# Kernel optimization log

Measured on AMD Instinct MI355X. Metric: run time of the kernel, lower is better.

The kernel has to match this reference:

```python
import jax, jax.numpy as jnp
import numpy as np


def setup_inputs() -> dict:
    key = jax.random.key(0)
    kx, kw = jax.random.split(key)
    x = jax.random.normal(kx, (8192, 4096), dtype=jnp.float32)
    weight = jax.random.normal(kw, (4096, 4096), dtype=jnp.float32)  # [out, in]
    return {"x": x, "weight": weight}


def reference(x, weight):
    sg = jax.lax.stop_gradient
    # --- ternary weight quantization with STE ---
    abs_mean = sg(jnp.mean(jnp.abs(weight)))           # detached scalar
    threshold = 0.7 * abs_mean
    w_quant = jnp.where(jnp.abs(weight) < threshold, 0.0, jnp.sign(weight))
    non_zero_mean = jnp.mean((w_quant != 0).astype(weight.dtype)) + 1e-8
    scale_w = abs_mean / non_zero_mean
    w_scaled = w_quant * scale_w
    w_ste = sg(w_scaled - weight) + weight
    # --- int8 activation quantization with STE ---
    q_max = 127.0
    x_abs_max = sg(jnp.max(jnp.abs(x)))
    scale_x = q_max / jnp.maximum(x_abs_max, 1e-12)    # guard div-by-zero; if x==0, output==0 anyway
    x_dequant = jnp.round(x * scale_x) / scale_x
    x_ste = sg(x_dequant - x) + x
    # --- full-precision GEMM on fake-quantized operands ---
    return jnp.einsum('ti,oi->to', x_ste, w_ste)  # [tokens, out]
```

## Files before the change

### kernel.cpp

```cpp
#include <hip/hip_runtime.h>
#include <stdint.h>


#define M_DIM 8192
#define N_DIM 4096
#define K_DIM 4096
#define W_ELEMS (N_DIM * K_DIM)
#define X_ELEMS (M_DIM * K_DIM)

typedef int   int4v   __attribute__((ext_vector_type(4)));
typedef float float4v __attribute__((ext_vector_type(4)));

#define WS_ABSMEAN 0
#define WS_SCALEX  4
#define WS_THR     8
#define WS_CS      16
#define WS_WSUM    64
#define WS_XMAX    16384
#define WS_NZ      24576
#define WS_WQ_OFF  32768
#define WS_XQ_OFF  (32768 + W_ELEMS)

__global__ __launch_bounds__(256) void pass1(const float4v* __restrict__ w,
                                             const float4v* __restrict__ x,
                                             uint8_t* ws) {
    const int tid = threadIdx.x;
    __shared__ double lsd[4];
    __shared__ float lsf[4];
    if (blockIdx.x < 1024) {
        int idx = blockIdx.x * 256 + tid;
        double s = 0.0;
#pragma unroll 4
        for (int it = 0; it < 16; ++it) {
            float4v v = w[idx + it * 262144];
            s += (double)fabsf(v.x) + (double)fabsf(v.y) + (double)fabsf(v.z) + (double)fabsf(v.w);
        }
        for (int off = 32; off > 0; off >>= 1) s += __shfl_down(s, off);
        if ((tid & 63) == 0) lsd[tid >> 6] = s;
        __syncthreads();
        if (tid == 0) ((double*)(ws + WS_WSUM))[blockIdx.x] = lsd[0] + lsd[1] + lsd[2] + lsd[3];
    } else {
        int b = blockIdx.x - 1024;
        int idx = b * 256 + tid;
        float m = 0.0f;
#pragma unroll 4
        for (int it = 0; it < 16; ++it) {
            float4v v = x[idx + it * 524288];
            m = fmaxf(m, fmaxf(fmaxf(fabsf(v.x), fabsf(v.y)), fmaxf(fabsf(v.z), fabsf(v.w))));
        }
        for (int off = 32; off > 0; off >>= 1) m = fmaxf(m, __shfl_down(m, off));
        if ((tid & 63) == 0) lsf[tid >> 6] = m;
        __syncthreads();
        if (tid == 0) ((float*)(ws + WS_XMAX))[b] = fmaxf(fmaxf(lsf[0], lsf[1]), fmaxf(lsf[2], lsf[3]));
    }
}

__global__ __launch_bounds__(256) void pass2(uint8_t* ws) {
    const int tid = threadIdx.x;
    const double* wp = (const double*)(ws + WS_WSUM);
    const float* xp = (const float*)(ws + WS_XMAX);
    double s = wp[tid] + wp[tid + 256] + wp[tid + 512] + wp[tid + 768];
    float m = 0.0f;
#pragma unroll
    for (int j = 0; j < 8; ++j) m = fmaxf(m, xp[tid + j * 256]);
    for (int off = 32; off > 0; off >>= 1) {
        s += __shfl_down(s, off);
        m = fmaxf(m, __shfl_down(m, off));
    }
    __shared__ double lsd[4];
    __shared__ float lsf[4];
    if ((tid & 63) == 0) { lsd[tid >> 6] = s; lsf[tid >> 6] = m; }
    __syncthreads();
    if (tid == 0) {
        double tot = lsd[0] + lsd[1] + lsd[2] + lsd[3];
        float maxAbs = fmaxf(fmaxf(lsf[0], lsf[1]), fmaxf(lsf[2], lsf[3]));
        float abs_mean = (float)(tot * (1.0 / 16777216.0));
        *(float*)(ws + WS_ABSMEAN) = abs_mean;
        *(float*)(ws + WS_SCALEX) = 127.0f / fmaxf(maxAbs, 1e-12f);
        *(float*)(ws + WS_THR) = 0.7f * abs_mean;
    }
}

__global__ __launch_bounds__(256) void quant(const float4v* __restrict__ w,
                                             const float4v* __restrict__ x,
                                             uint8_t* ws) {
    const int tid = threadIdx.x;
    uint32_t* wq = (uint32_t*)(ws + WS_WQ_OFF);
    uint32_t* xq = (uint32_t*)(ws + WS_XQ_OFF);
    if (blockIdx.x < 1024) {
        const float thr = *(const float*)(ws + WS_THR);
        int idx = blockIdx.x * 256 + tid;
        int nz = 0;
        for (int it = 0; it < 16; ++it) {
            int i = idx + it * 262144;
            float4v v = w[i];
            uint32_t pk = 0;
#pragma unroll
            for (int c = 0; c < 4; ++c) {
                float f = v[c];
                int q = (fabsf(f) < thr) ? 0 : (f > 0.0f ? 1 : -1);
                nz += (q != 0);
                pk |= (uint32_t)(q & 0xff) << (8 * c);
            }
            wq[i] = pk;
        }
        for (int off = 32; off > 0; off >>= 1) nz += __shfl_down(nz, off);
        __shared__ int lsn[4];
        if ((tid & 63) == 0) lsn[tid >> 6] = nz;
        __syncthreads();
        if (tid == 0) ((int*)(ws + WS_NZ))[blockIdx.x] = lsn[0] + lsn[1] + lsn[2] + lsn[3];
    } else {
        const float sx = *(const float*)(ws + WS_SCALEX);
        int b = blockIdx.x - 1024;
        int idx = b * 256 + tid;
        for (int it = 0; it < 16; ++it) {
            int i = idx + it * 524288;
            float4v v = x[i];
            uint32_t pk = 0;
#pragma unroll
            for (int c = 0; c < 4; ++c) {
                int q = (int)rintf(v[c] * sx);
                pk |= (uint32_t)(q & 0xff) << (8 * c);
            }
            xq[i] = pk;
        }
    }
}

__global__ __launch_bounds__(256) void pass3(uint8_t* ws) {
    const int tid = threadIdx.x;
    const int* np = (const int*)(ws + WS_NZ);
    int s = np[tid] + np[tid + 256] + np[tid + 512] + np[tid + 768];
    for (int off = 32; off > 0; off >>= 1) s += __shfl_down(s, off);
    __shared__ int ls[4];
    if ((tid & 63) == 0) ls[tid >> 6] = s;
    __syncthreads();
    if (tid == 0) {
        float nzm = (float)(ls[0] + ls[1] + ls[2] + ls[3]) * (1.0f / 16777216.0f) + 1e-8f;
        float abs_mean = *(const float*)(ws + WS_ABSMEAN);
        float sx = *(const float*)(ws + WS_SCALEX);
        *(float*)(ws + WS_CS) = (abs_mean / nzm) / sx;
    }
}

__device__ __forceinline__ void load16_to_lds(const void* gsrc, void* ldst) {
    __builtin_amdgcn_global_load_lds(
        (const __attribute__((address_space(1))) uint32_t*)gsrc,
        (__attribute__((address_space(3))) uint32_t*)ldst, 16, 0, 0);
}

__global__ __launch_bounds__(256) void gemm_i8(const int8_t* __restrict__ Aq,
                                               const int8_t* __restrict__ Bq,
                                               float* __restrict__ out,
                                               const uint8_t* __restrict__ ws) {
    __shared__ int8_t lds[32768];
    int8_t* ldsA = lds;
    int8_t* ldsB = lds + 16384;

    int bid = blockIdx.x;
    int cpx = gridDim.x >> 3;
    int swz = (bid & 7) * cpx + (bid >> 3);
    int bm = swz / (N_DIM / 128);
    int bn = swz % (N_DIM / 128);

    const int tid = threadIdx.x;
    const int lane = tid & 63;
    const int w = tid >> 6;
    const int wr = w >> 1, wc = w & 1;

    const int8_t* Abase = Aq + (size_t)bm * 128 * K_DIM;
    const int8_t* Bbase = Bq + (size_t)bn * 128 * K_DIM;

    int4v acc[4][4] = {};

    for (int kt = 0; kt < K_DIM; kt += 128) {
        __syncthreads();
#pragma unroll
        for (int i = 0; i < 4; ++i) {
            int p = i * 4096 + tid * 16;
            int r = p >> 7;
            int s = (p >> 4) & 7;
            int q = s ^ (r & 7);
            load16_to_lds(Abase + (size_t)r * K_DIM + kt + q * 16, ldsA + p);
            load16_to_lds(Bbase + (size_t)r * K_DIM + kt + q * 16, ldsB + p);
        }
        __syncthreads();

#pragma unroll
        for (int kh = 0; kh < 2; ++kh) {
            int4v af[4], bf[4];
            const int qq = kh * 4 + (lane >> 4);
#pragma unroll
            for (int m = 0; m < 4; ++m) {
                int rowA = wr * 64 + m * 16 + (lane & 15);
                af[m] = *(const int4v*)(ldsA + rowA * 128 + ((qq ^ (rowA & 7)) << 4));
            }
#pragma unroll
            for (int n = 0; n < 4; ++n) {
                int rowB = wc * 64 + n * 16 + (lane & 15);
                bf[n] = *(const int4v*)(ldsB + rowB * 128 + ((qq ^ (rowB & 7)) << 4));
            }
#pragma unroll
            for (int m = 0; m < 4; ++m)
#pragma unroll
                for (int n = 0; n < 4; ++n)
                    acc[m][n] = __builtin_amdgcn_mfma_i32_16x16x64_i8(af[m], bf[n], acc[m][n], 0, 0, 0);
        }
    }

    const float cs = *(const float*)(ws + WS_CS);

    const int orow0 = bm * 128 + wr * 64 + (lane >> 4) * 4;
    const int ocol0 = bn * 128 + wc * 64 + (lane & 15);
#pragma unroll
    for (int m = 0; m < 4; ++m)
#pragma unroll
        for (int n = 0; n < 4; ++n)
#pragma unroll
            for (int j = 0; j < 4; ++j) {
                int row = orow0 + m * 16 + j;
                int col = ocol0 + n * 16;
                out[(size_t)row * N_DIM + col] = (float)acc[m][n][j] * cs;
            }
}

extern "C" void kernel_launch(void* const* d_in, const int* in_sizes, int n_in,
                              void* d_out, int out_size, void* d_ws, size_t ws_size,
                              hipStream_t stream) {
    const float4v* x = (const float4v*)d_in[0];
    const float4v* wgt = (const float4v*)d_in[1];
    float* out = (float*)d_out;
    uint8_t* ws = (uint8_t*)d_ws;
    int8_t* wq = (int8_t*)(ws + WS_WQ_OFF);
    int8_t* xq = (int8_t*)(ws + WS_XQ_OFF);

    pass1<<<3072, 256, 0, stream>>>(wgt, x, ws);
    pass2<<<1, 256, 0, stream>>>(ws);
    quant<<<3072, 256, 0, stream>>>(wgt, x, ws);
    pass3<<<1, 256, 0, stream>>>(ws);
    gemm_i8<<<2048, 256, 0, stream>>>(xq, wq, out, ws);
}
```

Before: 488.3 us.

## Enlarge GEMM tiles, double-buffer LDS, and fold scalar reductions into consumer kernels

The int8 GEMM moves from 128x128 tiles with 256 threads to 256x256 tiles with 512 threads. K-tiles are double-buffered in LDS, prefetching the next tile while computing the current one, and MFMA bursts are bracketed with barriers and s_setprio. The two single-block scalar kernels are removed: each quant block re-reduces the per-block partials to get its threshold or scale, and each GEMM block recomputes the output scale. This removes launches and serialization and raises data reuse per tile, at the cost of redundant small reductions in every block and 128KB LDS per block, which limits occupancy.

```diff
diff --git a/kernel.cpp b/kernel.cpp
--- a/kernel.cpp
+++ b/kernel.cpp
@@ -5,94 +5,79 @@
 #define M_DIM 8192
 #define N_DIM 4096
 #define K_DIM 4096
-#define W_ELEMS (N_DIM * K_DIM)
-#define X_ELEMS (M_DIM * K_DIM)
 
 typedef int   int4v   __attribute__((ext_vector_type(4)));
 typedef float float4v __attribute__((ext_vector_type(4)));
 
-#define WS_ABSMEAN 0
-#define WS_SCALEX  4
-#define WS_THR     8
-#define WS_CS      16
-#define WS_WSUM    64
-#define WS_XMAX    16384
-#define WS_NZ      24576
-#define WS_WQ_OFF  32768
-#define WS_XQ_OFF  (32768 + W_ELEMS)
-
-__global__ __launch_bounds__(256) void pass1(const float4v* __restrict__ w,
-                                             const float4v* __restrict__ x,
-                                             uint8_t* ws) {
+#define WS_WSUM 64
+#define WS_XMAX 16448
+#define WS_NZ   32832
+#define WS_WQ   65536
+#define WS_XQ   (65536 + N_DIM * K_DIM)
+
+__global__ __launch_bounds__(256) void reduce_k(const float4v* __restrict__ w,
+                                                const float4v* __restrict__ x,
+                                                uint8_t* ws) {
     const int tid = threadIdx.x;
     __shared__ double lsd[4];
     __shared__ float lsf[4];
-    if (blockIdx.x < 1024) {
+    if (blockIdx.x < 2048) {
         int idx = blockIdx.x * 256 + tid;
-        double s = 0.0;
-#pragma unroll 4
-        for (int it = 0; it < 16; ++it) {
-            float4v v = w[idx + it * 262144];
-            s += (double)fabsf(v.x) + (double)fabsf(v.y) + (double)fabsf(v.z) + (double)fabsf(v.w);
-        }
+        double s0 = 0.0, s1 = 0.0;
+#pragma unroll
+        for (int it = 0; it < 8; it += 2) {
+            float4v a = w[idx + it * 524288];
+            float4v b = w[idx + (it + 1) * 524288];
+            s0 += (double)((fabsf(a.x) + fabsf(a.y)) + (fabsf(a.z) + fabsf(a.w)));
+            s1 += (double)((fabsf(b.x) + fabsf(b.y)) + (fabsf(b.z) + fabsf(b.w)));
+        }
+        double s = s0 + s1;
         for (int off = 32; off > 0; off >>= 1) s += __shfl_down(s, off);
         if ((tid & 63) == 0) lsd[tid >> 6] = s;
         __syncthreads();
         if (tid == 0) ((double*)(ws + WS_WSUM))[blockIdx.x] = lsd[0] + lsd[1] + lsd[2] + lsd[3];
     } else {
-        int b = blockIdx.x - 1024;
-        int idx = b * 256 + tid;
-        float m = 0.0f;
-#pragma unroll 4
-        for (int it = 0; it < 16; ++it) {
-            float4v v = x[idx + it * 524288];
-            m = fmaxf(m, fmaxf(fmaxf(fabsf(v.x), fabsf(v.y)), fmaxf(fabsf(v.z), fabsf(v.w))));
-        }
+        int idx = (blockIdx.x - 2048) * 256 + tid;
+        float m0 = 0.0f, m1 = 0.0f;
+#pragma unroll
+        for (int it = 0; it < 8; it += 2) {
+            float4v a = x[idx + it * 1048576];
+            float4v b = x[idx + (it + 1) * 1048576];
+            m0 = fmaxf(m0, fmaxf(fmaxf(fabsf(a.x), fabsf(a.y)), fmaxf(fabsf(a.z), fabsf(a.w))));
+            m1 = fmaxf(m1, fmaxf(fmaxf(fabsf(b.x), fabsf(b.y)), fmaxf(fabsf(b.z), fabsf(b.w))));
+        }
+        float m = fmaxf(m0, m1);
         for (int off = 32; off > 0; off >>= 1) m = fmaxf(m, __shfl_down(m, off));
         if ((tid & 63) == 0) lsf[tid >> 6] = m;
         __syncthreads();
-        if (tid == 0) ((float*)(ws + WS_XMAX))[b] = fmaxf(fmaxf(lsf[0], lsf[1]), fmaxf(lsf[2], lsf[3]));
-    }
-}
-
-__global__ __launch_bounds__(256) void pass2(uint8_t* ws) {
+        if (tid == 0)
+            ((float*)(ws + WS_XMAX))[blockIdx.x - 2048] = fmaxf(fmaxf(lsf[0], lsf[1]), fmaxf(lsf[2], lsf[3]));
+    }
+}
+
+__global__ __launch_bounds__(256) void quant_k(const float4v* __restrict__ w,
+                                               const float4v* __restrict__ x,
+                                               uint8_t* ws) {
     const int tid = threadIdx.x;
-    const double* wp = (const double*)(ws + WS_WSUM);
-    const float* xp = (const float*)(ws + WS_XMAX);
-    double s = wp[tid] + wp[tid + 256] + wp[tid + 512] + wp[tid + 768];
-    float m = 0.0f;
-#pragma unroll
-    for (int j = 0; j < 8; ++j) m = fmaxf(m, xp[tid + j * 256]);
-    for (int off = 32; off > 0; off >>= 1) {
-        s += __shfl_down(s, off);
-        m = fmaxf(m, __shfl_down(m, off));
-    }
     __shared__ double lsd[4];
     __shared__ float lsf[4];
-    if ((tid & 63) == 0) { lsd[tid >> 6] = s; lsf[tid >> 6] = m; }
-    __syncthreads();
-    if (tid == 0) {
-        double tot = lsd[0] + lsd[1] + lsd[2] + lsd[3];
-        float maxAbs = fmaxf(fmaxf(lsf[0], lsf[1]), fmaxf(lsf[2], lsf[3]));
-        float abs_mean = (float)(tot * (1.0 / 16777216.0));
-        *(float*)(ws + WS_ABSMEAN) = abs_mean;
-        *(float*)(ws + WS_SCALEX) = 127.0f / fmaxf(maxAbs, 1e-12f);
-        *(float*)(ws + WS_THR) = 0.7f * abs_mean;
-    }
-}
-
-__global__ __launch_bounds__(256) void quant(const float4v* __restrict__ w,
-                                             const float4v* __restrict__ x,
-                                             uint8_t* ws) {
-    const int tid = threadIdx.x;
-    uint32_t* wq = (uint32_t*)(ws + WS_WQ_OFF);
-    uint32_t* xq = (uint32_t*)(ws + WS_XQ_OFF);
-    if (blockIdx.x < 1024) {
-        const float thr = *(const float*)(ws + WS_THR);
+    __shared__ int lsn[4];
+    if (blockIdx.x < 2048) {
+        const double* wp = (const double*)(ws + WS_WSUM);
+        double s = 0.0;
+#pragma unroll
+        for (int j = 0; j < 8; ++j) s += wp[tid + j * 256];
+        for (int off = 32; off > 0; off >>= 1) s += __shfl_down(s, off);
+        if ((tid & 63) == 0) lsd[tid >> 6] = s;
+        __syncthreads();
+        const float thr = 0.7f * (float)((lsd[0] + lsd[1] + lsd[2] + lsd[3]) * (1.0 / 16777216.0));
+
+        uint32_t* wq = (uint32_t*)(ws + WS_WQ);
         int idx = blockIdx.x * 256 + tid;
         int nz = 0;
-        for (int it = 0; it < 16; ++it) {
-            int i = idx + it * 262144;
+#pragma unroll
+        for (int it = 0; it < 8; ++it) {
+            int i = idx + it * 524288;
             float4v v = w[i];
             uint32_t pk = 0;
 #pragma unroll
@@ -105,16 +90,25 @@
             wq[i] = pk;
         }
         for (int off = 32; off > 0; off >>= 1) nz += __shfl_down(nz, off);
-        __shared__ int lsn[4];
         if ((tid & 63) == 0) lsn[tid >> 6] = nz;
         __syncthreads();
         if (tid == 0) ((int*)(ws + WS_NZ))[blockIdx.x] = lsn[0] + lsn[1] + lsn[2] + lsn[3];
     } else {
-        const float sx = *(const float*)(ws + WS_SCALEX);
-        int b = blockIdx.x - 1024;
-        int idx = b * 256 + tid;
-        for (int it = 0; it < 16; ++it) {
-            int i = idx + it * 524288;
+        const float* xp = (const float*)(ws + WS_XMAX);
+        float m = 0.0f;
+#pragma unroll
+        for (int j = 0; j < 16; ++j) m = fmaxf(m, xp[tid + j * 256]);
+        for (int off = 32; off > 0; off >>= 1) m = fmaxf(m, __shfl_down(m, off));
+        if ((tid & 63) == 0) lsf[tid >> 6] = m;
+        __syncthreads();
+        const float maxAbs = fmaxf(fmaxf(lsf[0], lsf[1]), fmaxf(lsf[2], lsf[3]));
+        const float sx = 127.0f / fmaxf(maxAbs, 1e-12f);
+
+        uint32_t* xq = (uint32_t*)(ws + WS_XQ);
+        int idx = (blockIdx.x - 2048) * 256 + tid;
+#pragma unroll
+        for (int it = 0; it < 8; ++it) {
+            int i = idx + it * 1048576;
             float4v v = x[i];
             uint32_t pk = 0;
 #pragma unroll
@@ -124,22 +118,6 @@
             }
             xq[i] = pk;
         }
-    }
-}
-
-__global__ __launch_bounds__(256) void pass3(uint8_t* ws) {
-    const int tid = threadIdx.x;
-    const int* np = (const int*)(ws + WS_NZ);
-    int s = np[tid] + np[tid + 256] + np[tid + 512] + np[tid + 768];
-    for (int off = 32; off > 0; off >>= 1) s += __shfl_down(s, off);
-    __shared__ int ls[4];
-    if ((tid & 63) == 0) ls[tid >> 6] = s;
-    __syncthreads();
-    if (tid == 0) {
-        float nzm = (float)(ls[0] + ls[1] + ls[2] + ls[3]) * (1.0f / 16777216.0f) + 1e-8f;
-        float abs_mean = *(const float*)(ws + WS_ABSMEAN);
-        float sx = *(const float*)(ws + WS_SCALEX);
-        *(float*)(ws + WS_CS) = (abs_mean / nzm) / sx;
     }
 }
 
@@ -149,71 +127,129 @@
         (__attribute__((address_space(3))) uint32_t*)ldst, 16, 0, 0);
 }
 
-__global__ __launch_bounds__(256) void gemm_i8(const int8_t* __restrict__ Aq,
-                                               const int8_t* __restrict__ Bq,
-                                               float* __restrict__ out,
-                                               const uint8_t* __restrict__ ws) {
-    __shared__ int8_t lds[32768];
-    int8_t* ldsA = lds;
-    int8_t* ldsB = lds + 16384;
+__global__ __launch_bounds__(512, 2) void gemm_i8(const uint8_t* __restrict__ ws,
+                                                  float* __restrict__ out) {
+    alignas(16) __shared__ int8_t lds[131072];
+    __shared__ int nzw[8];
+    __shared__ float cs_sh;
+
+    const int tid = threadIdx.x;
+    const int lane = tid & 63;
+    const int w = tid >> 6;
+    const int wr = w >> 2, wc = w & 3;
+
+    const int8_t* Aq = (const int8_t*)(ws + WS_XQ);
+    const int8_t* Bq = (const int8_t*)(ws + WS_WQ);
+
+    {
+        const double* wp = (const double*)(ws + WS_WSUM);
+        const float* xp = (const float*)(ws + WS_XMAX);
+        const int* np = (const int*)(ws + WS_NZ);
+        double s = wp[tid] + wp[tid + 512] + wp[tid + 1024] + wp[tid + 1536];
+        float mx = 0.0f;
+#pragma unroll
+        for (int j = 0; j < 8; ++j) mx = fmaxf(mx, xp[tid + j * 512]);
+        int nv = np[tid] + np[tid + 512] + np[tid + 1024] + np[tid + 1536];
+        for (int off = 32; off > 0; off >>= 1) {
+            s += __shfl_down(s, off);
+            mx = fmaxf(mx, __shfl_down(mx, off));
+            nv += __shfl_down(nv, off);
+        }
+        __shared__ double sd[8];
+        __shared__ float sf[8];
+        if (lane == 0) { sd[w] = s; sf[w] = mx; nzw[w] = nv; }
+        __syncthreads();
+        if (tid == 0) {
+            double st = 0.0; float mt = 0.0f; int nt = 0;
+#pragma unroll
+            for (int j = 0; j < 8; ++j) { st += sd[j]; mt = fmaxf(mt, sf[j]); nt += nzw[j]; }
+            float abs_mean = (float)(st * (1.0 / 16777216.0));
+            float nzm = (float)nt * (1.0f / 16777216.0f) + 1e-8f;
+            float sx = 127.0f / fmaxf(mt, 1e-12f);
+            cs_sh = (abs_mean / nzm) / sx;
+        }
+        __syncthreads();
+    }
 
     int bid = blockIdx.x;
     int cpx = gridDim.x >> 3;
     int swz = (bid & 7) * cpx + (bid >> 3);
-    int bm = swz / (N_DIM / 128);
-    int bn = swz % (N_DIM / 128);
-
-    const int tid = threadIdx.x;
-    const int lane = tid & 63;
-    const int w = tid >> 6;
-    const int wr = w >> 1, wc = w & 1;
-
-    const int8_t* Abase = Aq + (size_t)bm * 128 * K_DIM;
-    const int8_t* Bbase = Bq + (size_t)bn * 128 * K_DIM;
-
-    int4v acc[4][4] = {};
-
-    for (int kt = 0; kt < K_DIM; kt += 128) {
-        __syncthreads();
+    int bm = swz >> 4;
+    int bn = swz & 15;
+
+    const int8_t* Abase = Aq + (size_t)bm * 256 * K_DIM;
+    const int8_t* Bbase = Bq + (size_t)bn * 256 * K_DIM;
+
+    auto stage = [&](int kt, int b) {
+        int8_t* dstA = lds + b * 65536;
+        int8_t* dstB = lds + b * 65536 + 32768;
 #pragma unroll
         for (int i = 0; i < 4; ++i) {
-            int p = i * 4096 + tid * 16;
+            int p = i * 8192 + tid * 16;
             int r = p >> 7;
-            int s = (p >> 4) & 7;
-            int q = s ^ (r & 7);
-            load16_to_lds(Abase + (size_t)r * K_DIM + kt + q * 16, ldsA + p);
-            load16_to_lds(Bbase + (size_t)r * K_DIM + kt + q * 16, ldsB + p);
-        }
-        __syncthreads();
-
-#pragma unroll
-        for (int kh = 0; kh < 2; ++kh) {
-            int4v af[4], bf[4];
-            const int qq = kh * 4 + (lane >> 4);
-#pragma unroll
-            for (int m = 0; m < 4; ++m) {
-                int rowA = wr * 64 + m * 16 + (lane & 15);
-                af[m] = *(const int4v*)(ldsA + rowA * 128 + ((qq ^ (rowA & 7)) << 4));
-            }
-#pragma unroll
-            for (int n = 0; n < 4; ++n) {
-                int rowB = wc * 64 + n * 16 + (lane & 15);
-                bf[n] = *(const int4v*)(ldsB + rowB * 128 + ((qq ^ (rowB & 7)) << 4));
-            }
-#pragma unroll
-            for (int m = 0; m < 4; ++m)
-#pragma unroll
-                for (int n = 0; n < 4; ++n)
-                    acc[m][n] = __builtin_amdgcn_mfma_i32_16x16x64_i8(af[m], bf[n], acc[m][n], 0, 0, 0);
-        }
-    }
-
-    const float cs = *(const float*)(ws + WS_CS);
-
-    const int orow0 = bm * 128 + wr * 64 + (lane >> 4) * 4;
-    const int ocol0 = bn * 128 + wc * 64 + (lane & 15);
-#pragma unroll
-    for (int m = 0; m < 4; ++m)
+            int q = ((p >> 4) & 7) ^ (r & 7);
+            load16_to_lds(Abase + (size_t)r * K_DIM + kt + q * 16, dstA + p);
+            load16_to_lds(Bbase + (size_t)r * K_DIM + kt + q * 16, dstB + p);
+        }
+    };
+
+    int4v acc[8][4] = {};
+
+    stage(0, 0);
+    const int rA0 = wr * 128 + (lane & 15);
+    const int rB0 = wc * 64 + (lane & 15);
+    const int lg = lane >> 4;
+    const int lx = lane & 7;
+
+    for (int t = 0; t < 32; ++t) {
+        const int cur = t & 1;
+        if (t < 31) {
+            stage((t + 1) * 128, cur ^ 1);
+            asm volatile("s_waitcnt vmcnt(8)" ::: "memory");
+        } else {
+            asm volatile("s_waitcnt vmcnt(0)" ::: "memory");
+        }
+        __builtin_amdgcn_s_barrier();
+
+        const int8_t* A = lds + cur * 65536;
+        const int8_t* B = lds + cur * 65536 + 32768;
+
+#pragma unroll
+        for (int kk = 0; kk < 2; ++kk) {
+            int4v bf[4];
+            const int slot = ((kk * 4 + lg) ^ lx) << 4;
+#pragma unroll
+            for (int mh = 0; mh < 2; ++mh) {
+                int4v af[4];
+                if (mh == 0) {
+#pragma unroll
+                    for (int n = 0; n < 4; ++n)
+                        bf[n] = *(const int4v*)(B + (rB0 + n * 16) * 128 + slot);
+                }
+#pragma unroll
+                for (int mi = 0; mi < 4; ++mi)
+                    af[mi] = *(const int4v*)(A + (rA0 + (mh * 4 + mi) * 16) * 128 + slot);
+
+                __builtin_amdgcn_s_barrier();
+                asm volatile("s_waitcnt lgkmcnt(0)" ::: "memory");
+                __builtin_amdgcn_s_setprio(1);
+#pragma unroll
+                for (int mi = 0; mi < 4; ++mi)
+#pragma unroll
+                    for (int n = 0; n < 4; ++n)
+                        acc[mh * 4 + mi][n] =
+                            __builtin_amdgcn_mfma_i32_16x16x64_i8(af[mi], bf[n], acc[mh * 4 + mi][n], 0, 0, 0);
+                __builtin_amdgcn_s_setprio(0);
+                __builtin_amdgcn_s_barrier();
+            }
+        }
+    }
+
+    const float cs = cs_sh;
+    const int orow0 = bm * 256 + wr * 128 + (lane >> 4) * 4;
+    const int ocol0 = bn * 256 + wc * 64 + (lane & 15);
+#pragma unroll
+    for (int m = 0; m < 8; ++m)
 #pragma unroll
         for (int n = 0; n < 4; ++n)
 #pragma unroll
@@ -231,12 +267,8 @@
     const float4v* wgt = (const float4v*)d_in[1];
     float* out = (float*)d_out;
     uint8_t* ws = (uint8_t*)d_ws;
-    int8_t* wq = (int8_t*)(ws + WS_WQ_OFF);
-    int8_t* xq = (int8_t*)(ws + WS_XQ_OFF);
-
-    pass1<<<3072, 256, 0, stream>>>(wgt, x, ws);
-    pass2<<<1, 256, 0, stream>>>(ws);
-    quant<<<3072, 256, 0, stream>>>(wgt, x, ws);
-    pass3<<<1, 256, 0, stream>>>(ws);
-    gemm_i8<<<2048, 256, 0, stream>>>(xq, wq, out, ws);
-}
+
+    reduce_k<<<6144, 256, 0, stream>>>(wgt, x, ws);
+    quant_k<<<6144, 256, 0, stream>>>(wgt, x, ws);
+    gemm_i8<<<512, 512, 0, stream>>>(ws, out);
+}
```

New measurement: 473.0 us. 3.1% less time.
